# Kernel tuning notes

Hardware: AMD Instinct MI355X
Metric: run time of the kernel (lower is better)

Reference implementation:

```python
import jax, jax.numpy as jnp
import numpy as np

HEATMAP_SIZE = 64

def _gauss5():
    n = np.array([[1, 4, 7, 4, 1],
                  [4, 16, 26, 16, 4],
                  [7, 26, 41, 26, 7],
                  [4, 16, 26, 16, 4],
                  [1, 4, 7, 4, 1]], dtype=np.float32) / 41.0
    return n

def setup_inputs() -> dict:
    key = jax.random.key(0)
    k1, k2, k3 = jax.random.split(key, 3)
    B, K = 1024, 24
    # coords in [-1.2, 1.2] so a few land out of the heatmap and exercise the masking path
    x = jax.random.uniform(k1, (B, K, 2), jnp.float32, -1.2, 1.2)
    # every (out,in) filter slice is the same 5x5 binomial gaussian (as in weights_init)
    weight = jnp.asarray(np.broadcast_to(_gauss5(), (K, K, 5, 5)).copy())
    vis_batch = jax.random.randint(k2, (256,), 0, B, jnp.int32)
    vis_kps = jax.random.randint(k3, (256,), 0, K, jnp.int32)
    return {"x": x, "weight": weight, "vis_batch": vis_batch, "vis_kps": vis_kps}

def _forward(x, weight, vis_batch, vis_kps):
    B, K, _ = x.shape
    H = HEATMAP_SIZE
    # j2d_resized = round((j2d + 1) / 2 * (H - 1)).long()
    coords = jnp.round((x + 1.0) * 0.5 * (H - 1)).astype(jnp.int32)  # [B,K,2] = (x,y)
    # rows with any out-of-range coord get both coords set to 0
    invalid = jnp.any((coords >= H) | (coords < 0), axis=-1)  # [B,K]
    coords = jnp.where(invalid[..., None], 0, coords)
    # torch quirk: only places a 1 where the x-coordinate is nonzero
    place = (coords[..., 0] != 0).astype(weight.dtype)  # [B,K]
    ohx = jax.nn.one_hot(coords[..., 0], H, dtype=weight.dtype)  # [B,K,H]
    ohy = jax.nn.one_hot(coords[..., 1], H, dtype=weight.dtype)  # [B,K,H]
    # sparse heatmap: 1 at (y, x)
    heat = place[..., None, None] * ohy[..., :, None] * ohx[..., None, :]  # [B,K,H,H]
    # heatmap[vis_batch, vis_kps, :, :] = 0
    kill = jnp.zeros((B, K), weight.dtype).at[vis_batch, vis_kps].set(1.0)
    heat = heat * (1.0 - kill)[..., None, None]
    # full 24->24 channel-mixing 5x5 conv, padding=2, no bias
    out = jax.lax.conv_general_dilated(
        heat, weight, window_strides=(1, 1), padding=((2, 2), (2, 2)),
        dimension_numbers=("NCHW", "OIHW", "NCHW"))
    return out

def reference(x, weight, vis_batch, vis_kps):
    return _forward(x, weight, vis_batch, vis_kps)
```

## Files before the change

### kernel.cpp

```cpp
#include <hip/hip_runtime.h>
#include <math.h>

#define B_SZ 1024
#define K_SZ 24
#define H_SZ 64
#define NVIS 256

typedef float vfloat4 __attribute__((ext_vector_type(4)));


__global__ __launch_bounds__(256) void gs_prep(
    const float2* __restrict__ x,
    const int*    __restrict__ vis_b,
    const int*    __restrict__ vis_k,
    int*          __restrict__ spike_tab)
{
    __shared__ unsigned char killf[256];
    const int tid  = threadIdx.x;
    const int base = blockIdx.x * 256;
    const int bk   = base + tid;
    killf[tid] = 0;

    const float2 c = x[bk];
    const int cx = (int)rintf((c.x + 1.0f) * 0.5f * 63.0f);
    const int cy = (int)rintf((c.y + 1.0f) * 0.5f * 63.0f);
    const bool ok = (cx >= 1) & (cx < H_SZ) & (cy >= 0) & (cy < H_SZ);
    int s = ok ? (cy * H_SZ + cx) : -1;

    const int code = vis_b[tid] * K_SZ + vis_k[tid];
    __syncthreads();
    const unsigned local = (unsigned)(code - base);
    if (local < 256u) killf[local] = 1;
    __syncthreads();
    if (killf[tid]) s = -1;
    spike_tab[bk] = s;
}

__global__ __launch_bounds__(256) void gs_main(
    const int*   __restrict__ spike_tab,
    const float* __restrict__ w,
    float*       __restrict__ out)
{
    __shared__ float tile[H_SZ * H_SZ];
    const int bid = blockIdx.x;
    const int b   = bid / K_SZ;
    const int o   = bid - b * K_SZ;
    const int tid = threadIdx.x;

    const int*   sp = spike_tab + b * K_SZ;
    const float* wo = w + o * (K_SZ * 25);
    int sv[3]; float wv[3]; int pp[3];
#pragma unroll
    for (int it = 0; it < 3; ++it) {
        const int t = tid + it * 256;
        sv[it] = -1;
        if (t < K_SZ * 25) {
            const int c = t / 25;
            pp[it] = t - c * 25;
            sv[it] = sp[c];
            wv[it] = wo[t];
        }
    }

    vfloat4* t4 = (vfloat4*)tile;
    const vfloat4 z = {0.f, 0.f, 0.f, 0.f};
#pragma unroll
    for (int r = 0; r < 4; ++r) t4[r * 256 + tid] = z;
    __syncthreads();

#pragma unroll
    for (int it = 0; it < 3; ++it) {
        const int s = sv[it];
        if (s >= 0) {
            const int y  = s >> 6;
            const int xx = s & 63;
            const int di = pp[it] / 5;
            const int dj = pp[it] - di * 5;
            const int i  = y + 2 - di;
            const int j  = xx + 2 - dj;
            if (((unsigned)i < H_SZ) & ((unsigned)j < H_SZ))
                atomicAdd(&tile[i * H_SZ + j], wv[it]);
        }
    }
    __syncthreads();

    vfloat4* o4 = (vfloat4*)(out + ((size_t)bid << 12));
#pragma unroll
    for (int r = 0; r < 4; ++r) {
        const int idx = r * 256 + tid;
        o4[idx] = t4[idx];
    }
}

extern "C" void kernel_launch(void* const* d_in, const int* in_sizes, int n_in,
                              void* d_out, int out_size, void* d_ws, size_t ws_size,
                              hipStream_t stream) {
    const float2* x     = (const float2*)d_in[0];
    const float*  w     = (const float*)d_in[1];
    const int*    vis_b = (const int*)d_in[2];
    const int*    vis_k = (const int*)d_in[3];
    float*        out   = (float*)d_out;
    int*          spike_tab = (int*)d_ws;

    gs_prep<<<(B_SZ * K_SZ) / 256, 256, 0, stream>>>(x, vis_b, vis_k, spike_tab);
    gs_main<<<B_SZ * K_SZ, 256, 0, stream>>>(spike_tab, w, out);
}
```

Baseline: 391.1 us.

## Split output tile into per-wave row bands to drop block barriers

Each 64-lane wavefront now owns a 16-row band of the 64x64 output tile. It reads the 24 spike codes through readlane broadcast and scatters only the taps that land in its band, so both __syncthreads calls go away. Each wave zeroes, accumulates and writes back its own band independently. In exchange every wave walks all 24 spikes serially with mostly idle lanes, where before the 600 taps were spread across all threads.

```diff
diff --git a/kernel.cpp b/kernel.cpp
--- a/kernel.cpp
+++ b/kernel.cpp
@@ -41,53 +41,51 @@
     const float* __restrict__ w,
     float*       __restrict__ out)
 {
-    __shared__ float tile[H_SZ * H_SZ];
-    const int bid = blockIdx.x;
-    const int b   = bid / K_SZ;
-    const int o   = bid - b * K_SZ;
-    const int tid = threadIdx.x;
+    __shared__ float tile[4][16 * H_SZ];
+    const int bid  = blockIdx.x;
+    const int b    = bid / K_SZ;
+    const int o    = bid - b * K_SZ;
+    const int tid  = threadIdx.x;
+    const int wv   = tid >> 6;
+    const int l    = tid & 63;
+    const int band = wv << 4;
 
-    const int*   sp = spike_tab + b * K_SZ;
+    float* t = tile[wv];
+
+    const int* sp = spike_tab + b * K_SZ;
+    const int myspike = (l < K_SZ) ? sp[l] : -1;
+
+    vfloat4* t4 = (vfloat4*)t;
+    const vfloat4 z = {0.f, 0.f, 0.f, 0.f};
+#pragma unroll
+    for (int r = 0; r < 4; ++r) t4[r * 64 + l] = z;
+
+    const int  di    = l / 5;
+    const int  dj    = l - di * 5;
+    const bool istap = (l < 25);
+
     const float* wo = w + o * (K_SZ * 25);
-    int sv[3]; float wv[3]; int pp[3];
+
 #pragma unroll
-    for (int it = 0; it < 3; ++it) {
-        const int t = tid + it * 256;
-        sv[it] = -1;
-        if (t < K_SZ * 25) {
-            const int c = t / 25;
-            pp[it] = t - c * 25;
-            sv[it] = sp[c];
-            wv[it] = wo[t];
+    for (int s = 0; s < K_SZ; ++s) {
+        const int code = __builtin_amdgcn_readlane(myspike, s);
+        if (code < 0) continue;
+        const int y = code >> 6;
+        if ((y + 2 < band) | (y - 2 >= band + 16)) continue;
+        const int x = code & 63;
+        const int i = y + 2 - di;
+        const int j = x + 2 - dj;
+        const unsigned ri = (unsigned)(i - band);
+        if (istap & (ri < 16u) & ((unsigned)j < (unsigned)H_SZ)) {
+            const float wt = wo[s * 25 + l];
+            atomicAdd(&t[ri * H_SZ + j], wt);
         }
     }
 
-    vfloat4* t4 = (vfloat4*)tile;
-    const vfloat4 z = {0.f, 0.f, 0.f, 0.f};
-#pragma unroll
-    for (int r = 0; r < 4; ++r) t4[r * 256 + tid] = z;
-    __syncthreads();
-
-#pragma unroll
-    for (int it = 0; it < 3; ++it) {
-        const int s = sv[it];
-        if (s >= 0) {
-            const int y  = s >> 6;
-            const int xx = s & 63;
-            const int di = pp[it] / 5;
-            const int dj = pp[it] - di * 5;
-            const int i  = y + 2 - di;
-            const int j  = xx + 2 - dj;
-            if (((unsigned)i < H_SZ) & ((unsigned)j < H_SZ))
-                atomicAdd(&tile[i * H_SZ + j], wv[it]);
-        }
-    }
-    __syncthreads();
-
-    vfloat4* o4 = (vfloat4*)(out + ((size_t)bid << 12));
+    vfloat4* o4 = (vfloat4*)(out + ((size_t)bid << 12) + (size_t)(band * H_SZ));
 #pragma unroll
     for (int r = 0; r < 4; ++r) {
-        const int idx = r * 256 + tid;
+        const int idx = r * 64 + l;
         o4[idx] = t4[idx];
     }
 }
```

Result: no change. 398.9 us (+2.0%).

## Fuse prep into main kernel and loop over output channels per batch block

Applied to the files above, without the earlier changes.

Removes the separate prep kernel and workspace table: each block now handles one batch item, computing its 24 spike positions and kill mask in shared memory, then loops over all 24 output channels, reusing the shared tile and zeroing it after each store. This removes one launch and the redundant per-channel spike loads. In exchange the grid shrinks from 24576 to 1024 blocks and adds two barriers per channel, which may reduce parallelism and latency hiding for a store-bound workload.

```diff
diff --git a/kernel.cpp b/kernel.cpp
--- a/kernel.cpp
+++ b/kernel.cpp
@@ -4,62 +4,29 @@
 #define B_SZ 1024
 #define K_SZ 24
 #define H_SZ 64
-#define NVIS 256
 
 typedef float vfloat4 __attribute__((ext_vector_type(4)));
 
 
-__global__ __launch_bounds__(256) void gs_prep(
+__global__ __launch_bounds__(256) void gs_batch(
     const float2* __restrict__ x,
+    const float*  __restrict__ w,
     const int*    __restrict__ vis_b,
     const int*    __restrict__ vis_k,
-    int*          __restrict__ spike_tab)
-{
-    __shared__ unsigned char killf[256];
-    const int tid  = threadIdx.x;
-    const int base = blockIdx.x * 256;
-    const int bk   = base + tid;
-    killf[tid] = 0;
-
-    const float2 c = x[bk];
-    const int cx = (int)rintf((c.x + 1.0f) * 0.5f * 63.0f);
-    const int cy = (int)rintf((c.y + 1.0f) * 0.5f * 63.0f);
-    const bool ok = (cx >= 1) & (cx < H_SZ) & (cy >= 0) & (cy < H_SZ);
-    int s = ok ? (cy * H_SZ + cx) : -1;
-
-    const int code = vis_b[tid] * K_SZ + vis_k[tid];
-    __syncthreads();
-    const unsigned local = (unsigned)(code - base);
-    if (local < 256u) killf[local] = 1;
-    __syncthreads();
-    if (killf[tid]) s = -1;
-    spike_tab[bk] = s;
-}
-
-__global__ __launch_bounds__(256) void gs_main(
-    const int*   __restrict__ spike_tab,
-    const float* __restrict__ w,
-    float*       __restrict__ out)
+    float*        __restrict__ out)
 {
     __shared__ float tile[H_SZ * H_SZ];
-    const int bid = blockIdx.x;
-    const int b   = bid / K_SZ;
-    const int o   = bid - b * K_SZ;
+    __shared__ int   spike[K_SZ];
+
+    const int b   = blockIdx.x;
     const int tid = threadIdx.x;
 
-    const int*   sp = spike_tab + b * K_SZ;
-    const float* wo = w + o * (K_SZ * 25);
-    int sv[3]; float wv[3]; int pp[3];
-#pragma unroll
-    for (int it = 0; it < 3; ++it) {
-        const int t = tid + it * 256;
-        sv[it] = -1;
-        if (t < K_SZ * 25) {
-            const int c = t / 25;
-            pp[it] = t - c * 25;
-            sv[it] = sp[c];
-            wv[it] = wo[t];
-        }
+    if (tid < K_SZ) {
+        const float2 c = x[b * K_SZ + tid];
+        const int cx = (int)rintf((c.x + 1.0f) * 0.5f * 63.0f);
+        const int cy = (int)rintf((c.y + 1.0f) * 0.5f * 63.0f);
+        const bool ok = (cx >= 1) & (cx < H_SZ) & (cy >= 0) & (cy < H_SZ);
+        spike[tid] = ok ? (cy * H_SZ + cx) : -1;
     }
 
     vfloat4* t4 = (vfloat4*)tile;
@@ -68,27 +35,58 @@
     for (int r = 0; r < 4; ++r) t4[r * 256 + tid] = z;
     __syncthreads();
 
-#pragma unroll
-    for (int it = 0; it < 3; ++it) {
-        const int s = sv[it];
-        if (s >= 0) {
-            const int y  = s >> 6;
-            const int xx = s & 63;
-            const int di = pp[it] / 5;
-            const int dj = pp[it] - di * 5;
-            const int i  = y + 2 - di;
-            const int j  = xx + 2 - dj;
-            if (((unsigned)i < H_SZ) & ((unsigned)j < H_SZ))
-                atomicAdd(&tile[i * H_SZ + j], wv[it]);
-        }
+    {
+        const int code = vis_b[tid] * K_SZ + vis_k[tid];
+        const unsigned local = (unsigned)(code - b * K_SZ);
+        if (local < (unsigned)K_SZ) spike[local] = -1;
     }
     __syncthreads();
 
-    vfloat4* o4 = (vfloat4*)(out + ((size_t)bid << 12));
+    int cc[3], di[3], dj[3]; bool act[3];
 #pragma unroll
-    for (int r = 0; r < 4; ++r) {
-        const int idx = r * 256 + tid;
-        o4[idx] = t4[idx];
+    for (int it = 0; it < 3; ++it) {
+        const int t = tid + it * 256;
+        act[it] = (t < K_SZ * 25);
+        const int c = t / 25;
+        const int p = t - c * 25;
+        cc[it] = c;
+        di[it] = p / 5;
+        dj[it] = p - (p / 5) * 5;
+    }
+
+    float* outb = out + (((size_t)b * K_SZ) << 12);
+
+    for (int o = 0; o < K_SZ; ++o) {
+        const float* wo = w + o * (K_SZ * 25);
+
+        float wv[3];
+#pragma unroll
+        for (int it = 0; it < 3; ++it)
+            if (act[it]) wv[it] = wo[tid + it * 256];
+
+#pragma unroll
+        for (int it = 0; it < 3; ++it) {
+            if (act[it]) {
+                const int s = spike[cc[it]];
+                if (s >= 0) {
+                    const int i = (s >> 6) + 2 - di[it];
+                    const int j = (s & 63) + 2 - dj[it];
+                    if (((unsigned)i < H_SZ) & ((unsigned)j < H_SZ))
+                        atomicAdd(&tile[i * H_SZ + j], wv[it]);
+                }
+            }
+        }
+        __syncthreads();
+
+        vfloat4* o4 = (vfloat4*)(outb + ((size_t)o << 12));
+#pragma unroll
+        for (int r = 0; r < 4; ++r) {
+            const int idx = r * 256 + tid;
+            const vfloat4 v = t4[idx];
+            o4[idx] = v;
+            t4[idx] = z;
+        }
+        __syncthreads();
     }
 }
 
@@ -100,8 +98,6 @@
     const int*    vis_b = (const int*)d_in[2];
     const int*    vis_k = (const int*)d_in[3];
     float*        out   = (float*)d_out;
-    int*          spike_tab = (int*)d_ws;
 
-    gs_prep<<<(B_SZ * K_SZ) / 256, 256, 0, stream>>>(x, vis_b, vis_k, spike_tab);
-    gs_main<<<B_SZ * K_SZ, 256, 0, stream>>>(spike_tab, w, out);
+    gs_batch<<<B_SZ, 256, 0, stream>>>(x, w, vis_b, vis_k, out);
 }
```

New measurement: 408.7 us. +4.5%, slower.
